# Performance work log

Measured on AMD Instinct MI355X. Metric: run time of the kernel, lower is better.

## Reference

```python
import jax, jax.numpy as jnp
import numpy as np

B, S, D, H = 4, 2048, 1024, 16
HD = D // H

def setup_inputs() -> dict:
    key = jax.random.key(0)
    ks = jax.random.split(key, 5)
    x = jax.random.normal(ks[0], (B, S, D), dtype=jnp.float32)
    mask = jnp.ones((B, S), dtype=jnp.int32)
    # torch nn.Linear init scale ~ 1/sqrt(fan_in); use small normal for stability
    qkv_w = jax.random.normal(ks[1], (3 * D, D), dtype=jnp.float32) * (1.0 / np.sqrt(D))
    qkv_b = jax.random.normal(ks[2], (3 * D,), dtype=jnp.float32) * 0.02
    out_w = jax.random.normal(ks[3], (D, D), dtype=jnp.float32) * (1.0 / np.sqrt(D))
    out_b = jax.random.normal(ks[4], (D,), dtype=jnp.float32) * 0.02
    return {"x": x, "mask": mask, "qkv_w": qkv_w, "qkv_b": qkv_b,
            "out_w": out_w, "out_b": out_b}

def reference(x, mask, qkv_w, qkv_b, out_w, out_b):
    b, s, d = x.shape
    scale = np.sqrt(HD).astype(np.float32)
    # qkv projection: torch Linear y = x @ W^T + b
    qkv = x @ qkv_w.T + qkv_b                      # (b, s, 3d)
    qkv = qkv.reshape(b, s, 3, H, HD)
    qkv = jnp.transpose(qkv, (2, 0, 3, 1, 4))      # (3, b, H, s, hd)
    q, k, v = qkv[0], qkv[1], qkv[2]
    scores = jnp.einsum('bhqd,bhkd->bhqk', q, k) / scale  # (b, H, s, s)
    neg_inf = jnp.float32(-jnp.inf)
    causal = jnp.tril(jnp.ones((s, s), dtype=bool))
    scores = jnp.where(causal[None, None], scores, neg_inf)
    key_mask = (mask != 0)[:, None, None, :]       # (b, 1, 1, s)
    scores = jnp.where(key_mask, scores, neg_inf)
    attn = jax.nn.softmax(scores, axis=-1)
    out = jnp.einsum('bhqk,bhkd->bhqd', attn, v)   # (b, H, s, hd)
    out = jnp.transpose(out, (0, 2, 1, 3)).reshape(b, s, d)
    return out @ out_w.T + out_b
```

## Files before the change

### kernel.cpp

```cpp
#include <hip/hip_runtime.h>
#include <stdint.h>
#include <type_traits>

#define BB  4
#define SS  2048
#define DD  1024
#define HH  16
#define HDD 64

typedef __attribute__((ext_vector_type(8))) short s16x8;
typedef __attribute__((ext_vector_type(4))) float f32x4;

__device__ inline short f2bf(float f) {
    union { float f; unsigned int u; } v; v.f = f;
    unsigned int r = (v.u + 0x7fffu + ((v.u >> 16) & 1u)) >> 16;
    return (short)r;
}

__device__ inline float bf2f(short s) {
    union { unsigned int u; float f; } v;
    v.u = ((unsigned int)(unsigned short)s) << 16;
    return v.f;
}

__device__ inline unsigned int pk2(float a, float b) {
    return (unsigned int)(unsigned short)f2bf(a) |
           ((unsigned int)(unsigned short)f2bf(b) << 16);
}

#define GLL(gp, lp) __builtin_amdgcn_global_load_lds( \
    (const __attribute__((address_space(1))) void*)(gp), \
    (__attribute__((address_space(3))) void*)(lp), 16, 0, 0)

__device__ inline void lds_barrier() {
    asm volatile("s_waitcnt lgkmcnt(0)" ::: "memory");
    __builtin_amdgcn_sched_barrier(0);
    __builtin_amdgcn_s_barrier();
    __builtin_amdgcn_sched_barrier(0);
}

__global__ void cvt_kernel(const float* __restrict__ src, short* __restrict__ dst, int n) {
    int i = (blockIdx.x * 256 + threadIdx.x) * 8;
    if (i >= n) return;
    const float4* s = (const float4*)(src + i);
    float4 a = s[0], b = s[1];
    s16x8 o;
    o[0]=f2bf(a.x); o[1]=f2bf(a.y); o[2]=f2bf(a.z); o[3]=f2bf(a.w);
    o[4]=f2bf(b.x); o[5]=f2bf(b.y); o[6]=f2bf(b.z); o[7]=f2bf(b.w);
    *(s16x8*)(dst + i) = o;
}

template<int EPI>
__global__ __launch_bounds__(256, 2)
void gemm128(const short* __restrict__ A, const short* __restrict__ Bw,
             const float* __restrict__ bias, float* __restrict__ Cf,
             short* __restrict__ Qo, short* __restrict__ Ko, short* __restrict__ Vo,
             int M, int N, int K, int nbx)
{
    __shared__ short lsA[2][128 * 64];
    __shared__ short lsB[2][128 * 64];

    const int tid  = threadIdx.x;
    const int w    = tid >> 6, lane = tid & 63;
    const int quad = lane >> 4, l15 = lane & 15;
    const int wm = w >> 1, wn = w & 1;
    const int cpx = gridDim.x >> 3;
    const int swz = (blockIdx.x & 7) * cpx + (blockIdx.x >> 3);
    const int m0 = (swz / nbx) * 128, n0 = (swz % nbx) * 128;
    const int grow = lane >> 3;
    const int gcol = ((lane & 7) ^ grow) * 8;
    const int l7 = l15 & 7;

    f32x4 acc[4][4] = {};

    auto issue = [&](int kt, int buf) {
#pragma unroll
        for (int jj = 0; jj < 4; ++jj) {
            int row = w * 32 + jj * 8 + grow;
            GLL(A + (size_t)(m0 + row) * K + kt * 64 + gcol,
                &lsA[buf][(w * 4 + jj) * 512]);
        }
#pragma unroll
        for (int jj = 0; jj < 4; ++jj) {
            int row = w * 32 + jj * 8 + grow;
            GLL(Bw + (size_t)(n0 + row) * K + kt * 64 + gcol,
                &lsB[buf][(w * 4 + jj) * 512]);
        }
    };

    const int NT = K >> 6;
    issue(0, 0);
    for (int t = 0; t < NT; ++t) {
        const int buf = t & 1;
        lds_barrier();
        if (t + 1 < NT) {
            issue(t + 1, buf ^ 1);
            asm volatile("s_waitcnt vmcnt(8)" ::: "memory");
        } else {
            asm volatile("s_waitcnt vmcnt(0)" ::: "memory");
        }
        __builtin_amdgcn_sched_barrier(0);
        __builtin_amdgcn_s_barrier();
        __builtin_amdgcn_sched_barrier(0);

        s16x8 af[4][2], bfr[4][2];
#pragma unroll
        for (int mf = 0; mf < 4; ++mf)
#pragma unroll
            for (int ks = 0; ks < 2; ++ks)
                af[mf][ks] = *(const s16x8*)&lsA[buf][(wm * 64 + mf * 16 + l15) * 64 +
                                                     (((ks * 4 + quad) ^ l7) * 8)];
#pragma unroll
        for (int nf = 0; nf < 4; ++nf)
#pragma unroll
            for (int ks = 0; ks < 2; ++ks)
                bfr[nf][ks] = *(const s16x8*)&lsB[buf][(wn * 64 + nf * 16 + l15) * 64 +
                                                      (((ks * 4 + quad) ^ l7) * 8)];

        __builtin_amdgcn_s_setprio(1);
#pragma unroll
        for (int ks = 0; ks < 2; ++ks)
#pragma unroll
            for (int mf = 0; mf < 4; ++mf)
#pragma unroll
                for (int nf = 0; nf < 4; ++nf)
                    acc[mf][nf] = __builtin_amdgcn_mfma_f32_16x16x32_bf16(
                                      af[mf][ks], bfr[nf][ks], acc[mf][nf], 0, 0, 0);
        __builtin_amdgcn_s_setprio(0);
    }

    if (EPI == 0) {
#pragma unroll
        for (int mf = 0; mf < 4; ++mf) {
            int row = m0 + wm * 64 + mf * 16 + quad * 4;
#pragma unroll
            for (int nf = 0; nf < 4; ++nf) {
                int col = n0 + wn * 64 + nf * 16 + l15;
                float bv = bias[col];
#pragma unroll
                for (int r = 0; r < 4; ++r)
                    Cf[(size_t)(row + r) * N + col] = acc[mf][nf][r] + bv;
            }
        }
    } else {
#pragma unroll
        for (int mf = 0; mf < 4; ++mf) {
            int row = m0 + wm * 64 + mf * 16 + quad * 4;
#pragma unroll
            for (int nf = 0; nf < 4; ++nf) {
                int col = n0 + wn * 64 + nf * 16 + l15;
                float bv = bias[col];
                int sel = col >> 10, h = (col >> 6) & 15, hd = col & 63;
#pragma unroll
                for (int r = 0; r < 4; ++r) {
                    int rr = row + r;
                    int b = rr >> 11, s = rr & 2047;
                    short val = f2bf(acc[mf][nf][r] + bv);
                    if (sel == 0)      Qo[(((size_t)b * HH + h) * SS + s) * HDD + hd] = val;
                    else if (sel == 1) Ko[(((size_t)b * HH + h) * SS + s) * HDD + hd] = val;
                    else               Vo[(((size_t)b * HH + h) * HDD + hd) * SS + s] = val;
                }
            }
        }
    }
}

__global__ __launch_bounds__(256, 2)
void attn_kernel(const short* __restrict__ Q, const short* __restrict__ Kb,
                 const short* __restrict__ Vb, const int* __restrict__ mask,
                 short* __restrict__ O)
{
    __shared__ short lsK[2][64 * 64];
    __shared__ short lsV[2][64 * 64];
    __shared__ short lsP[4][32 * 64];
    __shared__ short lsM[SS];

    const int tid  = threadIdx.x;
    const int w    = tid >> 6, lane = tid & 63;
    const int quad = lane >> 4, l15 = lane & 15;
    const int bx = blockIdx.x, bh = blockIdx.y;
    const int b = bh >> 4;
    const size_t baseQK = (size_t)bh * SS * HDD;
    const size_t baseV  = (size_t)bh * HDD * SS;
    const float SC = 0.18033688f;
    const int grow = lane >> 3;
    const int gcol = ((lane & 7) ^ grow) * 8;
    const int l7 = l15 & 7;

    {
        const int4* mp = (const int4*)(mask + b * SS);
        int4 a = mp[tid * 2], c = mp[tid * 2 + 1];
        const short NEG = f2bf(-1e30f);
        s16x8 mo;
        mo[0] = a.x ? (short)0 : NEG; mo[1] = a.y ? (short)0 : NEG;
        mo[2] = a.z ? (short)0 : NEG; mo[3] = a.w ? (short)0 : NEG;
        mo[4] = c.x ? (short)0 : NEG; mo[5] = c.y ? (short)0 : NEG;
        mo[6] = c.z ? (short)0 : NEG; mo[7] = c.w ? (short)0 : NEG;
        *(s16x8*)&lsM[tid * 8] = mo;
    }

    auto issue = [&](int kv0, int buf) {
#pragma unroll
        for (int jj = 0; jj < 2; ++jj) {
            int row = w * 16 + jj * 8 + grow;
            GLL(Kb + baseQK + (size_t)(kv0 + row) * HDD + gcol,
                &lsK[buf][(w * 2 + jj) * 512]);
        }
#pragma unroll
        for (int jj = 0; jj < 2; ++jj) {
            int row = w * 16 + jj * 8 + grow;
            GLL(Vb + baseV + (size_t)row * SS + kv0 + gcol,
                &lsV[buf][(w * 2 + jj) * 512]);
        }
    };

    for (int t = 0; t < 2; ++t) {
        const int qb = t ? bx : (15 - bx);
        const int q0 = qb * 128;
        const int qw0 = q0 + w * 32;

        s16x8 aq[2][2];
#pragma unroll
        for (int s = 0; s < 2; ++s)
#pragma unroll
            for (int ks = 0; ks < 2; ++ks)
                aq[s][ks] = *(const s16x8*)(Q + baseQK +
                    (size_t)(qw0 + s * 16 + l15) * HDD + ks * 32 + quad * 8);

        float m_r[2], l_r[2];
        f32x4 o_acc[2][4] = {};
#pragma unroll
        for (int s = 0; s < 2; ++s) { m_r[s] = -1e30f; l_r[s] = 0.f; }

        const int ntiles = 2 * qb + 2;

        lds_barrier();
        issue(0, 0);

        auto tile = [&](auto CC, int kv0, int buf, int kvn) {
            constexpr bool CAUS = decltype(CC)::value;

            lds_barrier();
            if (kvn >= 0) issue(kvn, buf ^ 1);

            float madd[4][4];
#pragma unroll
            for (int nt = 0; nt < 4; ++nt) {
                uint2 mw4 = *(const uint2*)&lsM[kv0 + nt * 16 + quad * 4];
                madd[nt][0] = bf2f((short)(mw4.x & 0xffff));
                madd[nt][1] = bf2f((short)(mw4.x >> 16));
                madd[nt][2] = bf2f((short)(mw4.y & 0xffff));
                madd[nt][3] = bf2f((short)(mw4.y >> 16));
            }

            if (kvn >= 0) asm volatile("s_waitcnt vmcnt(4)" ::: "memory");
            else          asm volatile("s_waitcnt vmcnt(0)" ::: "memory");
            __builtin_amdgcn_sched_barrier(0);
            __builtin_amdgcn_s_barrier();
            __builtin_amdgcn_sched_barrier(0);

            f32x4 sv[2][4];
#pragma unroll
            for (int s = 0; s < 2; ++s)
#pragma unroll
                for (int nt = 0; nt < 4; ++nt) sv[s][nt] = f32x4{};
#pragma unroll
            for (int ks = 0; ks < 2; ++ks)
#pragma unroll
                for (int nt = 0; nt < 4; ++nt) {
                    s16x8 kf = *(const s16x8*)&lsK[buf][(nt * 16 + l15) * 64 +
                                                       (((ks * 4 + quad) ^ l7) * 8)];
#pragma unroll
                    for (int s = 0; s < 2; ++s)
                        sv[s][nt] = __builtin_amdgcn_mfma_f32_16x16x32_bf16(
                                        kf, aq[s][ks], sv[s][nt], 0, 0, 0);
                }

#pragma unroll
            for (int s = 0; s < 2; ++s) {
                const int qg = qw0 + s * 16 + l15;
#pragma unroll
                for (int nt = 0; nt < 4; ++nt) {
                    const int kg0 = kv0 + nt * 16 + quad * 4;
#pragma unroll
                    for (int r = 0; r < 4; ++r) {
                        float scv = sv[s][nt][r] * SC + madd[nt][r];
                        if (CAUS && kg0 + r > qg) scv = -1e30f;
                        sv[s][nt][r] = scv;
                    }
                }
            }

            float rm[2];
#pragma unroll
            for (int s = 0; s < 2; ++s) {
                float v = fmaxf(fmaxf(fmaxf(sv[s][0][0], sv[s][0][1]),
                                      fmaxf(sv[s][0][2], sv[s][0][3])),
                                fmaxf(fmaxf(sv[s][1][0], sv[s][1][1]),
                                      fmaxf(sv[s][1][2], sv[s][1][3])));
                float v2 = fmaxf(fmaxf(fmaxf(sv[s][2][0], sv[s][2][1]),
                                       fmaxf(sv[s][2][2], sv[s][2][3])),
                                 fmaxf(fmaxf(sv[s][3][0], sv[s][3][1]),
                                       fmaxf(sv[s][3][2], sv[s][3][3])));
                v = fmaxf(v, v2);
                v = fmaxf(v, __shfl_xor(v, 16));
                v = fmaxf(v, __shfl_xor(v, 32));
                rm[s] = v;
            }
            float need = fmaxf(rm[0] - m_r[0], rm[1] - m_r[1]);
            if (!__all(need <= 8.0f)) {
#pragma unroll
                for (int s = 0; s < 2; ++s) {
                    float nm = fmaxf(m_r[s], rm[s]);
                    float al = __builtin_amdgcn_exp2f(m_r[s] - nm);
                    m_r[s] = nm;
                    l_r[s] *= al;
#pragma unroll
                    for (int r = 0; r < 4; ++r) {
                        float alq = __shfl(al, (quad << 2) + r + (lane & 48));
#pragma unroll
                        for (int ht = 0; ht < 4; ++ht)
                            o_acc[s][ht][r] *= alq;
                    }
                }
            }
#pragma unroll
            for (int s = 0; s < 2; ++s) {
                float rs = 0.f;
#pragma unroll
                for (int nt = 0; nt < 4; ++nt)
#pragma unroll
                    for (int r = 0; r < 4; ++r) {
                        float p = __builtin_amdgcn_exp2f(sv[s][nt][r] - m_r[s]);
                        sv[s][nt][r] = p;
                        rs += p;
                    }
                l_r[s] += rs;
            }

            short* lsPw = lsP[w];
#pragma unroll
            for (int s = 0; s < 2; ++s)
#pragma unroll
                for (int nt = 0; nt < 4; ++nt) {
                    uint2 pw;
                    pw.x = pk2(sv[s][nt][0], sv[s][nt][1]);
                    pw.y = pk2(sv[s][nt][2], sv[s][nt][3]);
                    int row = s * 16 + l15;
                    int g8 = (nt * 2 + (quad >> 1)) ^ l7;
                    *(uint2*)&lsPw[row * 64 + (g8 << 3) + ((quad & 1) << 2)] = pw;
                }
            asm volatile("s_waitcnt lgkmcnt(0)" ::: "memory");
            __builtin_amdgcn_sched_barrier(0);

            s16x8 ap[2][2];
#pragma unroll
            for (int s = 0; s < 2; ++s)
#pragma unroll
                for (int k2 = 0; k2 < 2; ++k2)
                    ap[s][k2] = *(const s16x8*)&lsPw[(s * 16 + l15) * 64 +
                                                     (((k2 * 4 + quad) ^ l7) << 3)];
#pragma unroll
            for (int ht = 0; ht < 4; ++ht)
#pragma unroll
                for (int k2 = 0; k2 < 2; ++k2) {
                    s16x8 vf = *(const s16x8*)&lsV[buf][(ht * 16 + l15) * 64 +
                                                        (((k2 * 4 + quad) ^ l7) * 8)];
#pragma unroll
                    for (int s = 0; s < 2; ++s)
                        o_acc[s][ht] = __builtin_amdgcn_mfma_f32_16x16x32_bf16(
                                           ap[s][k2], vf, o_acc[s][ht], 0, 0, 0);
                }
        };

        for (int kt = 0; kt < ntiles; ++kt) {
            const int kvn = (kt + 1 < ntiles) ? (kt + 1) * 64 : -1;
            if (kt >= 2 * qb) tile(std::true_type{},  kt * 64, kt & 1, kvn);
            else              tile(std::false_type{}, kt * 64, kt & 1, kvn);
        }

        const int hcol = (bh & 15) * HDD;
#pragma unroll
        for (int s = 0; s < 2; ++s) {
            float ls = l_r[s];
            ls += __shfl_xor(ls, 16);
            ls += __shfl_xor(ls, 32);
#pragma unroll
            for (int r = 0; r < 4; ++r) {
                float lq = __shfl(ls, (quad << 2) + r + (lane & 48));
                float inv = 1.0f / lq;
                int srow = qw0 + s * 16 + quad * 4 + r;
                size_t base = ((size_t)b * SS + srow) * DD + hcol;
#pragma unroll
                for (int ht = 0; ht < 4; ++ht)
                    O[base + ht * 16 + l15] = f2bf(o_acc[s][ht][r] * inv);
            }
        }
    }
}

extern "C" void kernel_launch(void* const* d_in, const int* in_sizes, int n_in,
                              void* d_out, int out_size, void* d_ws, size_t ws_size,
                              hipStream_t stream) {
    const float* x     = (const float*)d_in[0];
    const int*   mask  = (const int*)d_in[1];
    const float* qkv_w = (const float*)d_in[2];
    const float* qkv_b = (const float*)d_in[3];
    const float* out_w = (const float*)d_in[4];
    const float* out_b = (const float*)d_in[5];
    float* out = (float*)d_out;

    const size_t M1 = (size_t)BB * SS;
    short* ws  = (short*)d_ws;
    short* xb  = ws;
    short* qwb = xb  + M1 * DD;
    short* owb = qwb + (size_t)3 * DD * DD;
    short* Qb  = owb + (size_t)DD * DD;
    short* Kb  = Qb  + M1 * DD;
    short* Vb  = Kb  + M1 * DD;
    short* Ob  = Vb  + M1 * DD;

    cvt_kernel<<<(int)(M1 * DD / 8 / 256), 256, 0, stream>>>(x, xb, (int)(M1 * DD));
    cvt_kernel<<<3 * DD * DD / 8 / 256, 256, 0, stream>>>(qkv_w, qwb, 3 * DD * DD);
    cvt_kernel<<<DD * DD / 8 / 256, 256, 0, stream>>>(out_w, owb, DD * DD);

    gemm128<1><<<1536, 256, 0, stream>>>(xb, qwb, qkv_b, nullptr,
                                         Qb, Kb, Vb, 8192, 3072, 1024, 24);
    attn_kernel<<<dim3(8, BB * HH), 256, 0, stream>>>(Qb, Kb, Vb, mask, Ob);
    gemm128<0><<<512, 256, 0, stream>>>(Ob, owb, out_b, out,
                                        nullptr, nullptr, nullptr, 8192, 1024, 1024, 8);
}
```

Before: 292.1 us.

## Enlarge GEMM tiles to 256x256 with 8 waves and interleaved prefetch

Replaces the 128x128, 4-wave GEMM with a 256x256, 8-wave version that uses 128 KB of double-buffered LDS. Next-tile global loads are split into quarters and issued between sub-blocks of MFMA work, with barriers around each sub-block. The larger tile raises arithmetic intensity and cuts redundant global traffic. In exchange it launches far fewer blocks (128 for the output projection on a 256-CU part), adds more barriers per K step, and puts more pressure on registers and LDS occupancy.

Result: slower. 313.9 us (+7.5%).

```diff
diff --git a/kernel.cpp b/kernel.cpp
--- a/kernel.cpp
+++ b/kernel.cpp
@@ -51,101 +51,114 @@
 }
 
 template<int EPI>
-__global__ __launch_bounds__(256, 2)
-void gemm128(const short* __restrict__ A, const short* __restrict__ Bw,
+__global__ __launch_bounds__(512, 2)
+void gemm256(const short* __restrict__ A, const short* __restrict__ Bw,
              const float* __restrict__ bias, float* __restrict__ Cf,
              short* __restrict__ Qo, short* __restrict__ Ko, short* __restrict__ Vo,
              int M, int N, int K, int nbx)
 {
-    __shared__ short lsA[2][128 * 64];
-    __shared__ short lsB[2][128 * 64];
+    __shared__ short lsA[2][256 * 64];
+    __shared__ short lsB[2][256 * 64];
 
     const int tid  = threadIdx.x;
     const int w    = tid >> 6, lane = tid & 63;
     const int quad = lane >> 4, l15 = lane & 15;
-    const int wm = w >> 1, wn = w & 1;
+    const int wm = w >> 2, wn = w & 3;
     const int cpx = gridDim.x >> 3;
     const int swz = (blockIdx.x & 7) * cpx + (blockIdx.x >> 3);
-    const int m0 = (swz / nbx) * 128, n0 = (swz % nbx) * 128;
+    const int m0 = (swz / nbx) * 256, n0 = (swz % nbx) * 256;
     const int grow = lane >> 3;
     const int gcol = ((lane & 7) ^ grow) * 8;
     const int l7 = l15 & 7;
 
-    f32x4 acc[4][4] = {};
-
-    auto issue = [&](int kt, int buf) {
-#pragma unroll
-        for (int jj = 0; jj < 4; ++jj) {
-            int row = w * 32 + jj * 8 + grow;
-            GLL(A + (size_t)(m0 + row) * K + kt * 64 + gcol,
-                &lsA[buf][(w * 4 + jj) * 512]);
-        }
-#pragma unroll
-        for (int jj = 0; jj < 4; ++jj) {
-            int row = w * 32 + jj * 8 + grow;
-            GLL(Bw + (size_t)(n0 + row) * K + kt * 64 + gcol,
-                &lsB[buf][(w * 4 + jj) * 512]);
+    f32x4 acc[8][4] = {};
+
+    auto stage_half = [&](int kt, int p) {
+        const short* src = (p < 2) ? A : Bw;
+        const int g0 = ((p < 2) ? m0 : n0) + (p & 1) * 128;
+        short* dst = (p < 2) ? &lsA[kt & 1][(p & 1) * 128 * 64]
+                             : &lsB[kt & 1][(p & 1) * 128 * 64];
+#pragma unroll
+        for (int jj = 0; jj < 2; ++jj) {
+            int c = w * 2 + jj;
+            GLL(src + (size_t)(g0 + c * 8 + grow) * K + kt * 64 + gcol,
+                dst + c * 512);
         }
     };
 
     const int NT = K >> 6;
-    issue(0, 0);
-    for (int t = 0; t < NT; ++t) {
-        const int buf = t & 1;
-        lds_barrier();
-        if (t + 1 < NT) {
-            issue(t + 1, buf ^ 1);
-            asm volatile("s_waitcnt vmcnt(8)" ::: "memory");
-        } else {
-            asm volatile("s_waitcnt vmcnt(0)" ::: "memory");
-        }
+
+#pragma unroll
+    for (int p = 0; p < 4; ++p) stage_half(0, p);
+    asm volatile("s_waitcnt vmcnt(0)" ::: "memory");
+    __builtin_amdgcn_sched_barrier(0);
+    __builtin_amdgcn_s_barrier();
+    __builtin_amdgcn_sched_barrier(0);
+
+    for (int j = 0; j < NT; ++j) {
+        const int d = j & 1;
+
+        s16x8 bfr[4][2];
+#pragma unroll
+        for (int nf = 0; nf < 4; ++nf)
+#pragma unroll
+            for (int ks = 0; ks < 2; ++ks)
+                bfr[nf][ks] = *(const s16x8*)&lsB[d][(wn * 64 + nf * 16 + l15) * 64 +
+                                                    (((ks * 4 + quad) ^ l7) * 8)];
+
+#pragma unroll
+        for (int q = 0; q < 4; ++q) {
+            s16x8 af[2][2];
+#pragma unroll
+            for (int mf = 0; mf < 2; ++mf)
+#pragma unroll
+                for (int ks = 0; ks < 2; ++ks)
+                    af[mf][ks] = *(const s16x8*)&lsA[d][(wm * 128 + q * 32 + mf * 16 + l15) * 64 +
+                                                       (((ks * 4 + quad) ^ l7) * 8)];
+            if (j + 1 < NT) {
+                if (q == 0)      { stage_half(j + 1, 0); stage_half(j + 1, 1); }
+                else if (q == 1) { stage_half(j + 1, 2); stage_half(j + 1, 3); }
+            }
+            __builtin_amdgcn_s_barrier();
+            asm volatile("s_waitcnt lgkmcnt(0)" ::: "memory");
+            __builtin_amdgcn_sched_barrier(0);
+            __builtin_amdgcn_s_setprio(1);
+#pragma unroll
+            for (int ks = 0; ks < 2; ++ks)
+#pragma unroll
+                for (int mf = 0; mf < 2; ++mf)
+#pragma unroll
+                    for (int nf = 0; nf < 4; ++nf)
+                        acc[q * 2 + mf][nf] = __builtin_amdgcn_mfma_f32_16x16x32_bf16(
+                            af[mf][ks], bfr[nf][ks], acc[q * 2 + mf][nf], 0, 0, 0);
+            __builtin_amdgcn_s_setprio(0);
+            __builtin_amdgcn_s_barrier();
+            __builtin_amdgcn_sched_barrier(0);
+        }
+
+        asm volatile("s_waitcnt vmcnt(0)" ::: "memory");
         __builtin_amdgcn_sched_barrier(0);
         __builtin_amdgcn_s_barrier();
         __builtin_amdgcn_sched_barrier(0);
-
-        s16x8 af[4][2], bfr[4][2];
-#pragma unroll
-        for (int mf = 0; mf < 4; ++mf)
-#pragma unroll
-            for (int ks = 0; ks < 2; ++ks)
-                af[mf][ks] = *(const s16x8*)&lsA[buf][(wm * 64 + mf * 16 + l15) * 64 +
-                                                     (((ks * 4 + quad) ^ l7) * 8)];
-#pragma unroll
-        for (int nf = 0; nf < 4; ++nf)
-#pragma unroll
-            for (int ks = 0; ks < 2; ++ks)
-                bfr[nf][ks] = *(const s16x8*)&lsB[buf][(wn * 64 + nf * 16 + l15) * 64 +
-                                                      (((ks * 4 + quad) ^ l7) * 8)];
-
-        __builtin_amdgcn_s_setprio(1);
-#pragma unroll
-        for (int ks = 0; ks < 2; ++ks)
-#pragma unroll
-            for (int mf = 0; mf < 4; ++mf)
-#pragma unroll
-                for (int nf = 0; nf < 4; ++nf)
-                    acc[mf][nf] = __builtin_amdgcn_mfma_f32_16x16x32_bf16(
-                                      af[mf][ks], bfr[nf][ks], acc[mf][nf], 0, 0, 0);
-        __builtin_amdgcn_s_setprio(0);
     }
 
     if (EPI == 0) {
 #pragma unroll
-        for (int mf = 0; mf < 4; ++mf) {
-            int row = m0 + wm * 64 + mf * 16 + quad * 4;
+        for (int a = 0; a < 8; ++a) {
+            int row = m0 + wm * 128 + (a >> 1) * 32 + (a & 1) * 16 + quad * 4;
 #pragma unroll
             for (int nf = 0; nf < 4; ++nf) {
                 int col = n0 + wn * 64 + nf * 16 + l15;
                 float bv = bias[col];
 #pragma unroll
                 for (int r = 0; r < 4; ++r)
-                    Cf[(size_t)(row + r) * N + col] = acc[mf][nf][r] + bv;
+                    Cf[(size_t)(row + r) * N + col] = acc[a][nf][r] + bv;
             }
         }
     } else {
 #pragma unroll
-        for (int mf = 0; mf < 4; ++mf) {
-            int row = m0 + wm * 64 + mf * 16 + quad * 4;
+        for (int a = 0; a < 8; ++a) {
+            int row = m0 + wm * 128 + (a >> 1) * 32 + (a & 1) * 16 + quad * 4;
 #pragma unroll
             for (int nf = 0; nf < 4; ++nf) {
                 int col = n0 + wn * 64 + nf * 16 + l15;
@@ -155,7 +168,7 @@
                 for (int r = 0; r < 4; ++r) {
                     int rr = row + r;
                     int b = rr >> 11, s = rr & 2047;
-                    short val = f2bf(acc[mf][nf][r] + bv);
+                    short val = f2bf(acc[a][nf][r] + bv);
                     if (sel == 0)      Qo[(((size_t)b * HH + h) * SS + s) * HDD + hd] = val;
                     else if (sel == 1) Ko[(((size_t)b * HH + h) * SS + s) * HDD + hd] = val;
                     else               Vo[(((size_t)b * HH + h) * HDD + hd) * SS + s] = val;
@@ -424,9 +437,9 @@
     cvt_kernel<<<3 * DD * DD / 8 / 256, 256, 0, stream>>>(qkv_w, qwb, 3 * DD * DD);
     cvt_kernel<<<DD * DD / 8 / 256, 256, 0, stream>>>(out_w, owb, DD * DD);
 
-    gemm128<1><<<1536, 256, 0, stream>>>(xb, qwb, qkv_b, nullptr,
-                                         Qb, Kb, Vb, 8192, 3072, 1024, 24);
+    gemm256<1><<<384, 512, 0, stream>>>(xb, qwb, qkv_b, nullptr,
+                                        Qb, Kb, Vb, 8192, 3072, 1024, 12);
     attn_kernel<<<dim3(8, BB * HH), 256, 0, stream>>>(Qb, Kb, Vb, mask, Ob);
-    gemm128<0><<<512, 256, 0, stream>>>(Ob, owb, out_b, out,
-                                        nullptr, nullptr, nullptr, 8192, 1024, 1024, 8);
-}
+    gemm256<0><<<128, 512, 0, stream>>>(Ob, owb, out_b, out,
+                                        nullptr, nullptr, nullptr, 8192, 1024, 1024, 4);
+}
```
